# Kernel optimization log

Measured on AMD Instinct MI355X. Metric: run time of the kernel, lower is better.

## Reference

```python
import jax, jax.numpy as jnp
import numpy as np

N_NODES = 100000
N_EDGES = 800000
IN_FEATS = 128
HIDDEN = 64
SCALE = 0.5 ** 0.5  # sqrt(0.5) residual scale
BN_EPS = 1e-5


def setup_inputs() -> dict:
    key = jax.random.key(0)
    ks = jax.random.split(key, 12)
    return {
        "src": jax.random.randint(ks[0], (N_EDGES,), 0, N_NODES, dtype=jnp.int64)
        if jax.config.jax_enable_x64 else jax.random.randint(ks[0], (N_EDGES,), 0, N_NODES),
        "dst": jax.random.randint(ks[1], (N_EDGES,), 0, N_NODES),
        "x": jax.random.normal(ks[2], (N_NODES, IN_FEATS), dtype=jnp.float32),
        "fc_w": jax.random.normal(ks[3], (IN_FEATS, HIDDEN), dtype=jnp.float32) * 0.05,
        "fc_b": jax.random.normal(ks[4], (HIDDEN,), dtype=jnp.float32) * 0.05,
        "w1": jax.random.normal(ks[5], (HIDDEN, HIDDEN), dtype=jnp.float32) * 0.05,
        "b1": jax.random.normal(ks[6], (HIDDEN,), dtype=jnp.float32) * 0.05,
        "w2": jax.random.normal(ks[7], (HIDDEN, HIDDEN), dtype=jnp.float32) * 0.05,
        "b2": jax.random.normal(ks[8], (HIDDEN,), dtype=jnp.float32) * 0.05,
        "gamma": jax.random.normal(ks[9], (HIDDEN,), dtype=jnp.float32) * 0.05 + 1.0,
        "beta": jax.random.normal(ks[10], (HIDDEN,), dtype=jnp.float32) * 0.05,
    }


def _graph_conv(h, w, b, src, dst, norm_src, norm_dst, n_nodes):
    # DGL GraphConv, norm='both': y = D_in^{-1/2} A D_out^{-1/2} (h W) + b
    h = h @ w                                   # [N, H]
    m = h[src] * norm_src[:, None]              # gather + src-degree norm, [E, H]
    agg = jax.ops.segment_sum(m, dst, num_segments=n_nodes)  # scatter-add, [N, H]
    return agg * norm_dst[:, None] + b


def reference(src, dst, x, fc_w, fc_b, w1, b1, w2, b2, gamma, beta):
    n_nodes = x.shape[0]
    ones_e = jnp.ones(src.shape[0], dtype=x.dtype)
    deg_out = jnp.clip(jax.ops.segment_sum(ones_e, src, num_segments=n_nodes), 1.0)
    deg_in = jnp.clip(jax.ops.segment_sum(ones_e, dst, num_segments=n_nodes), 1.0)
    norm_src = (deg_out ** -0.5)[src]           # per-edge source normalization
    norm_dst = deg_in ** -0.5                   # per-node destination normalization

    h = x @ fc_w + fc_b                          # fc: [N, H]
    h = (h + _graph_conv(h, w1, b1, src, dst, norm_src, norm_dst, n_nodes)) * SCALE
    h = (h + _graph_conv(h, w2, b2, src, dst, norm_src, norm_dst, n_nodes)) * SCALE

    # BatchNorm1d (training-mode batch statistics over nodes, biased variance)
    mu = h.mean(axis=0)
    var = ((h - mu) ** 2).mean(axis=0)
    h = (h - mu) * jax.lax.rsqrt(var + BN_EPS) * gamma + beta
    return h
```

## Files before the change

kernel.cpp:

```cpp
#include <hip/hip_runtime.h>

#define HIDDEN 64
#define INFEAT 128
#define SCALE_C 0.70710678118654752f
#define BN_EPS 1e-5f
#define AGG_GRID 2048
#define RED_BLK 32

__device__ __forceinline__ int rli(int v, int l){ return __builtin_amdgcn_readlane(v, l); }

__device__ __forceinline__ void hist_body(int bid, const int* __restrict__ src,
    const int* __restrict__ dst, int* __restrict__ degO, int* __restrict__ degI,
    int* __restrict__ rank, int E){
  int e = bid * 256 + threadIdx.x;
  if (e < E){
    atomicAdd(&degO[src[e]], 1);
    rank[e] = atomicAdd(&degI[dst[e]], 1);
  }
}

__device__ __forceinline__ void place_body(int bid, const int* __restrict__ src,
    const int* __restrict__ dst, const int* __restrict__ rank,
    const int* __restrict__ rp, int* __restrict__ cs, int E){
  int e = bid * 256 + threadIdx.x;
  if (e < E){
    cs[rp[dst[e]] + rank[e]] = src[e];
  }
}

template<int KDIM, bool ADDB, bool SCALEROW>
__device__ __forceinline__ void gemm_body(int bid, const float* __restrict__ X,
    const float* __restrict__ W, const float* __restrict__ B,
    float* __restrict__ Y, const float* __restrict__ nrm, int N)
{
  __shared__ float xl[128 * 33];
  const int tid  = threadIdx.x;
  const int lane = tid & 63;
  const int wid  = __builtin_amdgcn_readfirstlane(tid >> 6);
  const int nodehalf = wid >> 1;
  const int c0 = (wid & 1) * 32;
  const int base = bid * 128;
  const int myNode = nodehalf * 64 + lane;
  const int gnode = base + myNode;

  float acc[32];
  #pragma unroll
  for (int c = 0; c < 32; ++c) acc[c] = ADDB ? B[c0 + c] : 0.f;

  constexpr int NCHUNK = KDIM / 32;
  #pragma unroll 1
  for (int ck = 0; ck < NCHUNK; ++ck){
    __syncthreads();
    #pragma unroll
    for (int i = 0; i < 4; ++i){
      int f  = i * 256 + tid;
      int nd = f >> 3;
      int kq = f & 7;
      float4 v = make_float4(0.f, 0.f, 0.f, 0.f);
      if (base + nd < N)
        v = *(const float4*)(X + (size_t)(base + nd) * KDIM + ck * 32 + kq * 4);
      float* p = &xl[nd * 33 + kq * 4];
      p[0] = v.x; p[1] = v.y; p[2] = v.z; p[3] = v.w;
    }
    __syncthreads();
    const float* wrow = W + (size_t)ck * 32 * HIDDEN + c0;
    #pragma unroll
    for (int k = 0; k < 32; ++k){
      float xv = xl[myNode * 33 + k];
      #pragma unroll
      for (int c = 0; c < 32; ++c)
        acc[c] = fmaf(xv, wrow[k * HIDDEN + c], acc[c]);
    }
  }

  if (gnode < N){
    float sc = SCALEROW ? nrm[gnode] : 1.f;
    float4* yp = (float4*)(Y + (size_t)gnode * HIDDEN + c0);
    #pragma unroll
    for (int j = 0; j < 8; ++j)
      yp[j] = make_float4(acc[4*j]*sc, acc[4*j+1]*sc, acc[4*j+2]*sc, acc[4*j+3]*sc);
  }
}

__device__ __forceinline__ int role_gemm_idx(int b, int GB, int TOT, int& histIdx){
  int fb  = (int)(((long)b * GB) / TOT);
  int fb1 = (int)(((long)(b + 1) * GB) / TOT);
  histIdx = b - fb;
  return (fb1 > fb) ? fb : -1;
}

__global__ __launch_bounds__(256) void k_mega1(const int* __restrict__ src,
    const int* __restrict__ dst, int* __restrict__ degO, int* __restrict__ degI,
    int* __restrict__ rank, int E,
    const float* __restrict__ x, const float* __restrict__ fc_w,
    const float* __restrict__ fc_b, float* __restrict__ h, int N, int GB, int TOT){
  int hIdx;
  int g = role_gemm_idx(blockIdx.x, GB, TOT, hIdx);
  if (g >= 0) gemm_body<INFEAT, true, false>(g, x, fc_w, fc_b, h, nullptr, N);
  else        hist_body(hIdx, src, dst, degO, degI, rank, E);
}

__global__ __launch_bounds__(256) void k_mega2(const int* __restrict__ src,
    const int* __restrict__ dst, const int* __restrict__ rank,
    const int* __restrict__ rp, int* __restrict__ cs, int E,
    const float* __restrict__ h, const float* __restrict__ w1,
    float* __restrict__ t, const float* __restrict__ norm_out, int N, int GB, int TOT){
  int hIdx;
  int g = role_gemm_idx(blockIdx.x, GB, TOT, hIdx);
  if (g >= 0) gemm_body<HIDDEN, false, true>(g, h, w1, nullptr, t, norm_out, N);
  else        place_body(hIdx, src, dst, rank, rp, cs, E);
}

__global__ __launch_bounds__(256) void k_gemm64(const float* __restrict__ X,
    const float* __restrict__ W, float* __restrict__ Y,
    const float* __restrict__ nrm, int N){
  gemm_body<HIDDEN, false, true>(blockIdx.x, X, W, nullptr, Y, nrm, N);
}

__global__ void k_scan1(const int* __restrict__ deg, int* __restrict__ bsum, int N){
  __shared__ int sh[256];
  int t = threadIdx.x;
  int i = blockIdx.x * 256 + t;
  sh[t] = (i < N) ? deg[i] : 0;
  __syncthreads();
  for (int ofs = 128; ofs > 0; ofs >>= 1){
    if (t < ofs) sh[t] += sh[t + ofs];
    __syncthreads();
  }
  if (t == 0) bsum[blockIdx.x] = sh[0];
}

__global__ void k_scan2(int* __restrict__ bsum, int NB){
  __shared__ int sh[512];
  int t = threadIdx.x;
  int v = (t < NB) ? bsum[t] : 0;
  sh[t] = v;
  __syncthreads();
  for (int ofs = 1; ofs < 512; ofs <<= 1){
    int u = (t >= ofs) ? sh[t - ofs] : 0;
    __syncthreads();
    sh[t] += u;
    __syncthreads();
  }
  if (t < NB) bsum[t] = sh[t] - v;
}

__global__ void k_scan3(const int* __restrict__ degI, const int* __restrict__ degO,
                        const int* __restrict__ bofs, int* __restrict__ rp,
                        float* __restrict__ norm_out, float* __restrict__ norm_in,
                        int N, int E){
  __shared__ int sh[256];
  int t = threadIdx.x;
  int i = blockIdx.x * 256 + t;
  int v = (i < N) ? degI[i] : 0;
  sh[t] = v;
  __syncthreads();
  for (int ofs = 1; ofs < 256; ofs <<= 1){
    int u = (t >= ofs) ? sh[t - ofs] : 0;
    __syncthreads();
    sh[t] += u;
    __syncthreads();
  }
  if (i < N){
    int excl = sh[t] - v + bofs[blockIdx.x];
    rp[i] = excl;
    if (i == N - 1) rp[N] = E;
    norm_out[i] = rsqrtf((float)max(degO[i], 1));
    norm_in[i]  = rsqrtf((float)max(v, 1));
  }
}

__device__ __forceinline__ float gather_row(const int* __restrict__ rp,
    const int* __restrict__ cs, const float* __restrict__ t, int n, int lane){
  const int start = rp[n], end = rp[n + 1];
  float acc = 0.f;
  for (int j0 = start; j0 < end; j0 += 64){
    int cnt = end - j0; if (cnt > 64) cnt = 64;
    int sidx = (j0 + lane < end) ? cs[j0 + lane] : 0;
    int d = 0;
    for (; d + 8 <= cnt; d += 8){
      int a0 = rli(sidx, d),   a1 = rli(sidx, d+1);
      int a2 = rli(sidx, d+2), a3 = rli(sidx, d+3);
      int a4 = rli(sidx, d+4), a5 = rli(sidx, d+5);
      int a6 = rli(sidx, d+6), a7 = rli(sidx, d+7);
      float v0 = t[(size_t)a0 * HIDDEN + lane];
      float v1 = t[(size_t)a1 * HIDDEN + lane];
      float v2 = t[(size_t)a2 * HIDDEN + lane];
      float v3 = t[(size_t)a3 * HIDDEN + lane];
      float v4 = t[(size_t)a4 * HIDDEN + lane];
      float v5 = t[(size_t)a5 * HIDDEN + lane];
      float v6 = t[(size_t)a6 * HIDDEN + lane];
      float v7 = t[(size_t)a7 * HIDDEN + lane];
      acc += v0; acc += v1; acc += v2; acc += v3;
      acc += v4; acc += v5; acc += v6; acc += v7;
    }
    for (; d < cnt; ++d)
      acc += t[(size_t)rli(sidx, d) * HIDDEN + lane];
  }
  return acc;
}

template<bool BN>
__global__ __launch_bounds__(256) void k_agg(const int* __restrict__ rp, const int* __restrict__ cs,
    const float* __restrict__ t, const float* __restrict__ norm_in,
    const float* __restrict__ b, float* __restrict__ h, float* __restrict__ bnpart, int N)
{
  const int tid = threadIdx.x;
  const int lane = tid & 63;
  const int wv = (blockIdx.x * 256 + tid) >> 6;
  const int nw = (gridDim.x * 256) >> 6;
  const float bv = b[lane];
  float s1 = 0.f, s2 = 0.f;

  for (int n = wv; n < N; n += nw){
    float acc = gather_row(rp, cs, t, n, lane);
    size_t idx = (size_t)n * HIDDEN + lane;
    float v = (h[idx] + acc * norm_in[n] + bv) * SCALE_C;
    h[idx] = v;
    if (BN){ s1 += v; s2 += v * v; }
  }

  if (BN){
    __shared__ float l1[256], l2[256];
    l1[tid] = s1; l2[tid] = s2;
    __syncthreads();
    if (tid < 64){
      float a1 = l1[tid] + l1[tid+64] + l1[tid+128] + l1[tid+192];
      float a2 = l2[tid] + l2[tid+64] + l2[tid+128] + l2[tid+192];
      bnpart[blockIdx.x * 128 + tid] = a1;
      bnpart[blockIdx.x * 128 + 64 + tid] = a2;
    }
  }
}

__global__ __launch_bounds__(256) void k_bnred(const float* __restrict__ bnpart,
    float* __restrict__ bnred, int nblk){
  int col  = threadIdx.x & 127;
  int half = threadIdx.x >> 7;
  int rows = nblk / RED_BLK;
  int r0 = blockIdx.x * rows;
  float s = 0.f;
  for (int r = half; r < rows; r += 2)
    s += bnpart[(size_t)(r0 + r) * 128 + col];
  __shared__ float sh[256];
  sh[threadIdx.x] = s;
  __syncthreads();
  if (threadIdx.x < 128)
    bnred[blockIdx.x * 128 + threadIdx.x] = sh[threadIdx.x] + sh[threadIdx.x + 128];
}

__global__ void k_bnfin(const float* __restrict__ bnred,
    const float* __restrict__ gamma, const float* __restrict__ beta,
    float* __restrict__ bnab, float invN){
  int c = threadIdx.x;
  float s1 = 0.f, s2 = 0.f;
  #pragma unroll
  for (int b = 0; b < RED_BLK; ++b){ s1 += bnred[b*128 + c]; s2 += bnred[b*128 + 64 + c]; }
  float mu  = s1 * invN;
  float var = s2 * invN - mu * mu;
  float rstd = rsqrtf(var + BN_EPS);
  float sc = gamma[c] * rstd;
  bnab[c] = sc;
  bnab[64 + c] = beta[c] - mu * sc;
}

__global__ void k_bnapply(float* __restrict__ h, const float* __restrict__ bnab, long total4){
  long i = (long)blockIdx.x * blockDim.x + threadIdx.x;
  if (i < total4){
    int c = (int)((i * 4) & 63);
    float4 v = ((float4*)h)[i];
    v.x = fmaf(v.x, bnab[c],     bnab[64 + c]);
    v.y = fmaf(v.y, bnab[c + 1], bnab[65 + c]);
    v.z = fmaf(v.z, bnab[c + 2], bnab[66 + c]);
    v.w = fmaf(v.w, bnab[c + 3], bnab[67 + c]);
    ((float4*)h)[i] = v;
  }
}

extern "C" void kernel_launch(void* const* d_in, const int* in_sizes, int n_in,
                              void* d_out, int out_size, void* d_ws, size_t ws_size,
                              hipStream_t stream){
  const int* src = (const int*)d_in[0];
  const int* dst = (const int*)d_in[1];
  const float* x     = (const float*)d_in[2];
  const float* fc_w  = (const float*)d_in[3];
  const float* fc_b  = (const float*)d_in[4];
  const float* w1    = (const float*)d_in[5];
  const float* b1    = (const float*)d_in[6];
  const float* w2    = (const float*)d_in[7];
  const float* b2    = (const float*)d_in[8];
  const float* gamma = (const float*)d_in[9];
  const float* beta  = (const float*)d_in[10];
  const int E = in_sizes[0];
  const int N = in_sizes[2] / INFEAT;
  const int NB = (N + 255) / 256;
  const int EB = (E + 255) / 256;
  const int GB = (N + 127) / 128;
  const int TOT = EB + GB;

  float* h = (float*)d_out;

  float* t        = (float*)d_ws;
  float* norm_out = t + (size_t)N * HIDDEN;
  float* norm_in  = norm_out + N;
  float* bnpart   = norm_in + N;
  float* bnred    = bnpart + AGG_GRID * 128;
  float* bnab     = bnred + RED_BLK * 128;
  int*   degO     = (int*)(bnab + 128);
  int*   degI     = degO + N;
  int*   rp       = degI + N;
  int*   bsum     = rp + N + 1;
  int*   rank     = bsum + 512;
  int*   cs       = rank + E;

  hipMemsetAsync(degO, 0, 2 * (size_t)N * sizeof(int), stream);

  k_mega1<<<TOT, 256, 0, stream>>>(src, dst, degO, degI, rank, E,
                                   x, fc_w, fc_b, h, N, GB, TOT);

  k_scan1<<<NB, 256, 0, stream>>>(degI, bsum, N);
  k_scan2<<<1, 512, 0, stream>>>(bsum, NB);
  k_scan3<<<NB, 256, 0, stream>>>(degI, degO, bsum, rp, norm_out, norm_in, N, E);

  k_mega2<<<TOT, 256, 0, stream>>>(src, dst, rank, rp, cs, E,
                                   h, w1, t, norm_out, N, GB, TOT);

  k_agg<false><<<AGG_GRID, 256, 0, stream>>>(rp, cs, t, norm_in, b1, h, nullptr, N);

  k_gemm64<<<GB, 256, 0, stream>>>(h, w2, t, norm_out, N);
  k_agg<true><<<AGG_GRID, 256, 0, stream>>>(rp, cs, t, norm_in, b2, h, bnpart, N);

  k_bnred<<<RED_BLK, 256, 0, stream>>>(bnpart, bnred, AGG_GRID);
  k_bnfin<<<1, 64, 0, stream>>>(bnred, gamma, beta, bnab, 1.0f / (float)N);
  long total4 = (long)N * HIDDEN / 4;
  k_bnapply<<<(int)((total4 + 255) / 256), 256, 0, stream>>>(h, bnab, total4);
}
```

Before: 374.8 us.

## Fuse the conv1 weight GEMM into the fc GEMM and apply source norm during gather

The fc GEMM now keeps its output tile in shared memory and immediately multiplies it by w1, writing both h and t. This removes the separate pass that re-read h to produce t. Out-degree counting moves out of the first kernel into the placement kernel, which runs after the scan. The per-source normalization is no longer applied to t at GEMM time; it is recomputed as rsqrt(degO) for every edge inside the aggregation gather, for both conv layers. In exchange, the gather does an extra degO load and rsqrt per neighbour, and the larger shared-memory tile may lower occupancy of the mixed histogram/GEMM kernel.

New measurement: 370.4 us. About the same (-1.2%).

```diff
diff --git a/kernel.cpp b/kernel.cpp
--- a/kernel.cpp
+++ b/kernel.cpp
@@ -9,31 +9,12 @@
 
 __device__ __forceinline__ int rli(int v, int l){ return __builtin_amdgcn_readlane(v, l); }
 
-__device__ __forceinline__ void hist_body(int bid, const int* __restrict__ src,
-    const int* __restrict__ dst, int* __restrict__ degO, int* __restrict__ degI,
-    int* __restrict__ rank, int E){
-  int e = bid * 256 + threadIdx.x;
-  if (e < E){
-    atomicAdd(&degO[src[e]], 1);
-    rank[e] = atomicAdd(&degI[dst[e]], 1);
-  }
-}
-
-__device__ __forceinline__ void place_body(int bid, const int* __restrict__ src,
-    const int* __restrict__ dst, const int* __restrict__ rank,
-    const int* __restrict__ rp, int* __restrict__ cs, int E){
-  int e = bid * 256 + threadIdx.x;
-  if (e < E){
-    cs[rp[dst[e]] + rank[e]] = src[e];
-  }
-}
-
-template<int KDIM, bool ADDB, bool SCALEROW>
+template<int KDIM, bool ADDB, bool FUSET>
 __device__ __forceinline__ void gemm_body(int bid, const float* __restrict__ X,
     const float* __restrict__ W, const float* __restrict__ B,
-    float* __restrict__ Y, const float* __restrict__ nrm, int N)
+    float* __restrict__ Y, const float* __restrict__ W2, float* __restrict__ T, int N)
 {
-  __shared__ float xl[128 * 33];
+  __shared__ float smem[128 * 65];
   const int tid  = threadIdx.x;
   const int lane = tid & 63;
   const int wid  = __builtin_amdgcn_readfirstlane(tid >> 6);
@@ -59,14 +40,14 @@
       float4 v = make_float4(0.f, 0.f, 0.f, 0.f);
       if (base + nd < N)
         v = *(const float4*)(X + (size_t)(base + nd) * KDIM + ck * 32 + kq * 4);
-      float* p = &xl[nd * 33 + kq * 4];
+      float* p = &smem[nd * 33 + kq * 4];
       p[0] = v.x; p[1] = v.y; p[2] = v.z; p[3] = v.w;
     }
     __syncthreads();
     const float* wrow = W + (size_t)ck * 32 * HIDDEN + c0;
     #pragma unroll
     for (int k = 0; k < 32; ++k){
-      float xv = xl[myNode * 33 + k];
+      float xv = smem[myNode * 33 + k];
       #pragma unroll
       for (int c = 0; c < 32; ++c)
         acc[c] = fmaf(xv, wrow[k * HIDDEN + c], acc[c]);
@@ -74,11 +55,35 @@
   }
 
   if (gnode < N){
-    float sc = SCALEROW ? nrm[gnode] : 1.f;
     float4* yp = (float4*)(Y + (size_t)gnode * HIDDEN + c0);
     #pragma unroll
     for (int j = 0; j < 8; ++j)
-      yp[j] = make_float4(acc[4*j]*sc, acc[4*j+1]*sc, acc[4*j+2]*sc, acc[4*j+3]*sc);
+      yp[j] = make_float4(acc[4*j], acc[4*j+1], acc[4*j+2], acc[4*j+3]);
+  }
+
+  if constexpr (FUSET){
+    __syncthreads();
+    #pragma unroll
+    for (int c = 0; c < 32; ++c)
+      smem[myNode * 65 + c0 + c] = acc[c];
+    __syncthreads();
+    float tacc[32];
+    #pragma unroll
+    for (int c = 0; c < 32; ++c) tacc[c] = 0.f;
+    const float* w2r = W2 + c0;
+    #pragma unroll
+    for (int k = 0; k < 64; ++k){
+      float hv = smem[myNode * 65 + k];
+      #pragma unroll
+      for (int c = 0; c < 32; ++c)
+        tacc[c] = fmaf(hv, w2r[k * HIDDEN + c], tacc[c]);
+    }
+    if (gnode < N){
+      float4* tp = (float4*)(T + (size_t)gnode * HIDDEN + c0);
+      #pragma unroll
+      for (int j = 0; j < 8; ++j)
+        tp[j] = make_float4(tacc[4*j], tacc[4*j+1], tacc[4*j+2], tacc[4*j+3]);
+    }
   }
 }
 
@@ -89,32 +94,33 @@
   return (fb1 > fb) ? fb : -1;
 }
 
-__global__ __launch_bounds__(256) void k_mega1(const int* __restrict__ src,
-    const int* __restrict__ dst, int* __restrict__ degO, int* __restrict__ degI,
-    int* __restrict__ rank, int E,
+__global__ __launch_bounds__(256) void k_mega1(const int* __restrict__ dst,
+    int* __restrict__ degI, int* __restrict__ rank, int E,
     const float* __restrict__ x, const float* __restrict__ fc_w,
-    const float* __restrict__ fc_b, float* __restrict__ h, int N, int GB, int TOT){
+    const float* __restrict__ fc_b, float* __restrict__ h,
+    const float* __restrict__ w1, float* __restrict__ t, int N, int GB, int TOT){
   int hIdx;
   int g = role_gemm_idx(blockIdx.x, GB, TOT, hIdx);
-  if (g >= 0) gemm_body<INFEAT, true, false>(g, x, fc_w, fc_b, h, nullptr, N);
-  else        hist_body(hIdx, src, dst, degO, degI, rank, E);
-}
-
-__global__ __launch_bounds__(256) void k_mega2(const int* __restrict__ src,
+  if (g >= 0) gemm_body<INFEAT, true, true>(g, x, fc_w, fc_b, h, w1, t, N);
+  else {
+    int e = hIdx * 256 + threadIdx.x;
+    if (e < E) rank[e] = atomicAdd(&degI[dst[e]], 1);
+  }
+}
+
+__global__ __launch_bounds__(256) void k_place2(const int* __restrict__ src,
     const int* __restrict__ dst, const int* __restrict__ rank,
-    const int* __restrict__ rp, int* __restrict__ cs, int E,
-    const float* __restrict__ h, const float* __restrict__ w1,
-    float* __restrict__ t, const float* __restrict__ norm_out, int N, int GB, int TOT){
-  int hIdx;
-  int g = role_gemm_idx(blockIdx.x, GB, TOT, hIdx);
-  if (g >= 0) gemm_body<HIDDEN, false, true>(g, h, w1, nullptr, t, norm_out, N);
-  else        place_body(hIdx, src, dst, rank, rp, cs, E);
+    const int* __restrict__ rp, int* __restrict__ cs, int* __restrict__ degO, int E){
+  int e = (blockIdx.x >> 1) * 256 + threadIdx.x;
+  if (e < E){
+    if (blockIdx.x & 1) atomicAdd(&degO[src[e]], 1);
+    else                cs[rp[dst[e]] + rank[e]] = src[e];
+  }
 }
 
 __global__ __launch_bounds__(256) void k_gemm64(const float* __restrict__ X,
-    const float* __restrict__ W, float* __restrict__ Y,
-    const float* __restrict__ nrm, int N){
-  gemm_body<HIDDEN, false, true>(blockIdx.x, X, W, nullptr, Y, nrm, N);
+    const float* __restrict__ W, float* __restrict__ Y, int N){
+  gemm_body<HIDDEN, false, false>(blockIdx.x, X, W, nullptr, Y, nullptr, nullptr, N);
 }
 
 __global__ void k_scan1(const int* __restrict__ deg, int* __restrict__ bsum, int N){
@@ -145,10 +151,8 @@
   if (t < NB) bsum[t] = sh[t] - v;
 }
 
-__global__ void k_scan3(const int* __restrict__ degI, const int* __restrict__ degO,
-                        const int* __restrict__ bofs, int* __restrict__ rp,
-                        float* __restrict__ norm_out, float* __restrict__ norm_in,
-                        int N, int E){
+__global__ void k_scan3(const int* __restrict__ degI, const int* __restrict__ bofs,
+                        int* __restrict__ rp, float* __restrict__ norm_in, int N, int E){
   __shared__ int sh[256];
   int t = threadIdx.x;
   int i = blockIdx.x * 256 + t;
@@ -165,13 +169,13 @@
     int excl = sh[t] - v + bofs[blockIdx.x];
     rp[i] = excl;
     if (i == N - 1) rp[N] = E;
-    norm_out[i] = rsqrtf((float)max(degO[i], 1));
-    norm_in[i]  = rsqrtf((float)max(v, 1));
+    norm_in[i] = rsqrtf((float)max(v, 1));
   }
 }
 
 __device__ __forceinline__ float gather_row(const int* __restrict__ rp,
-    const int* __restrict__ cs, const float* __restrict__ t, int n, int lane){
+    const int* __restrict__ cs, const float* __restrict__ t,
+    const int* __restrict__ degO, int n, int lane){
   const int start = rp[n], end = rp[n + 1];
   float acc = 0.f;
   for (int j0 = start; j0 < end; j0 += 64){
@@ -191,19 +195,32 @@
       float v5 = t[(size_t)a5 * HIDDEN + lane];
       float v6 = t[(size_t)a6 * HIDDEN + lane];
       float v7 = t[(size_t)a7 * HIDDEN + lane];
-      acc += v0; acc += v1; acc += v2; acc += v3;
-      acc += v4; acc += v5; acc += v6; acc += v7;
-    }
-    for (; d < cnt; ++d)
-      acc += t[(size_t)rli(sidx, d) * HIDDEN + lane];
+      float n0 = rsqrtf((float)degO[a0]);
+      float n1 = rsqrtf((float)degO[a1]);
+      float n2 = rsqrtf((float)degO[a2]);
+      float n3 = rsqrtf((float)degO[a3]);
+      float n4 = rsqrtf((float)degO[a4]);
+      float n5 = rsqrtf((float)degO[a5]);
+      float n6 = rsqrtf((float)degO[a6]);
+      float n7 = rsqrtf((float)degO[a7]);
+      acc = fmaf(v0, n0, acc); acc = fmaf(v1, n1, acc);
+      acc = fmaf(v2, n2, acc); acc = fmaf(v3, n3, acc);
+      acc = fmaf(v4, n4, acc); acc = fmaf(v5, n5, acc);
+      acc = fmaf(v6, n6, acc); acc = fmaf(v7, n7, acc);
+    }
+    for (; d < cnt; ++d){
+      int a = rli(sidx, d);
+      acc = fmaf(t[(size_t)a * HIDDEN + lane], rsqrtf((float)degO[a]), acc);
+    }
   }
   return acc;
 }
 
 template<bool BN>
 __global__ __launch_bounds__(256) void k_agg(const int* __restrict__ rp, const int* __restrict__ cs,
-    const float* __restrict__ t, const float* __restrict__ norm_in,
-    const float* __restrict__ b, float* __restrict__ h, float* __restrict__ bnpart, int N)
+    const float* __restrict__ t, const int* __restrict__ degO,
+    const float* __restrict__ norm_in, const float* __restrict__ b,
+    float* __restrict__ h, float* __restrict__ bnpart, int N)
 {
   const int tid = threadIdx.x;
   const int lane = tid & 63;
@@ -213,7 +230,7 @@
   float s1 = 0.f, s2 = 0.f;
 
   for (int n = wv; n < N; n += nw){
-    float acc = gather_row(rp, cs, t, n, lane);
+    float acc = gather_row(rp, cs, t, degO, n, lane);
     size_t idx = (size_t)n * HIDDEN + lane;
     float v = (h[idx] + acc * norm_in[n] + bv) * SCALE_C;
     h[idx] = v;
@@ -301,8 +318,7 @@
   float* h = (float*)d_out;
 
   float* t        = (float*)d_ws;
-  float* norm_out = t + (size_t)N * HIDDEN;
-  float* norm_in  = norm_out + N;
+  float* norm_in  = t + (size_t)N * HIDDEN;
   float* bnpart   = norm_in + N;
   float* bnred    = bnpart + AGG_GRID * 128;
   float* bnab     = bnred + RED_BLK * 128;
@@ -315,20 +331,19 @@
 
   hipMemsetAsync(degO, 0, 2 * (size_t)N * sizeof(int), stream);
 
-  k_mega1<<<TOT, 256, 0, stream>>>(src, dst, degO, degI, rank, E,
-                                   x, fc_w, fc_b, h, N, GB, TOT);
+  k_mega1<<<TOT, 256, 0, stream>>>(dst, degI, rank, E,
+                                   x, fc_w, fc_b, h, w1, t, N, GB, TOT);
 
   k_scan1<<<NB, 256, 0, stream>>>(degI, bsum, N);
   k_scan2<<<1, 512, 0, stream>>>(bsum, NB);
-  k_scan3<<<NB, 256, 0, stream>>>(degI, degO, bsum, rp, norm_out, norm_in, N, E);
-
-  k_mega2<<<TOT, 256, 0, stream>>>(src, dst, rank, rp, cs, E,
-                                   h, w1, t, norm_out, N, GB, TOT);
-
-  k_agg<false><<<AGG_GRID, 256, 0, stream>>>(rp, cs, t, norm_in, b1, h, nullptr, N);
-
-  k_gemm64<<<GB, 256, 0, stream>>>(h, w2, t, norm_out, N);
-  k_agg<true><<<AGG_GRID, 256, 0, stream>>>(rp, cs, t, norm_in, b2, h, bnpart, N);
+  k_scan3<<<NB, 256, 0, stream>>>(degI, bsum, rp, norm_in, N, E);
+
+  k_place2<<<2 * EB, 256, 0, stream>>>(src, dst, rank, rp, cs, degO, E);
+
+  k_agg<false><<<AGG_GRID, 256, 0, stream>>>(rp, cs, t, degO, norm_in, b1, h, nullptr, N);
+
+  k_gemm64<<<GB, 256, 0, stream>>>(h, w2, t, N);
+  k_agg<true><<<AGG_GRID, 256, 0, stream>>>(rp, cs, t, degO, norm_in, b2, h, bnpart, N);
 
   k_bnred<<<RED_BLK, 256, 0, stream>>>(bnpart, bnred, AGG_GRID);
   k_bnfin<<<1, 64, 0, stream>>>(bnred, gamma, beta, bnab, 1.0f / (float)N);
```
